# Optimization experiments

Measured on AMD Instinct MI355X. Metric: run time of the kernel, lower is better.

## Reference

```python
import jax, jax.numpy as jnp
import numpy as np

B, L, D = 32, 8192, 1024
KERNEL = 5
PAD = (KERNEL - 1) // 2
UNIT = 2
TOPK = 100  # min(max_num_moments=100, L)


def setup_inputs() -> dict:
    key = jax.random.key(0)
    ks = jax.random.split(key, 8)
    scale = 1.0 / np.sqrt(D)
    return {
        "x": jax.random.normal(ks[0], (B, L, D), dtype=jnp.float32),
        "saliency": jax.random.normal(ks[1], (B, L), dtype=jnp.float32),
        "Wc": jax.random.normal(ks[2], (D, 1), dtype=jnp.float32) * scale,
        "bc": jnp.zeros((1,), dtype=jnp.float32),
        "Ww": jax.random.normal(ks[3], (D, 1), dtype=jnp.float32) * scale,
        "bw": jnp.zeros((1,), dtype=jnp.float32),
        "Wo": jax.random.normal(ks[4], (D, 1), dtype=jnp.float32) * scale,
        "bo": jnp.zeros((1,), dtype=jnp.float32),
    }


def _get_boundary(center_pred, window_pred, offset_pred):
    # center_pred: [B, L]. CenterNet-style 1D NMS: keep only local maxima.
    hmax = jax.lax.reduce_window(
        center_pred, -jnp.inf, jax.lax.max,
        window_dimensions=(1, KERNEL), window_strides=(1, 1),
        padding=[(0, 0), (PAD, PAD)])
    cp = center_pred * (hmax == center_pred).astype(center_pred.dtype)
    scores, inds = jax.lax.top_k(cp, TOPK)                    # [B, K]
    off = jnp.take_along_axis(offset_pred, inds, axis=1)      # [B, K]
    win = jnp.clip(jnp.take_along_axis(window_pred, inds, axis=1), 0.0, None)
    center = jnp.clip(inds.astype(cp.dtype) + off, 0.0, float(L - 1))
    start = jnp.clip(center - win * 0.5, 0.0, float(L - 1)) * UNIT
    end = jnp.clip(center + win * 0.5, 0.0, float(L - 1)) * UNIT + UNIT
    return jnp.stack([start, end, scores], axis=-1)           # [B, K, 3]


def reference(x, saliency, Wc, bc, Ww, bw, Wo, bo):
    mask = (saliency >= 0).astype(x.dtype)                    # [B, L]
    center_pred = jax.nn.sigmoid(jnp.squeeze(x @ Wc + bc, -1)) * mask
    window_pred = jnp.squeeze(x @ Ww + bw, -1)
    offset_pred = jnp.squeeze(x @ Wo + bo, -1)
    return _get_boundary(center_pred, window_pred, offset_pred)
```

## Files before the change

kernel.cpp:

```cpp
#include <hip/hip_runtime.h>
#include <stdint.h>

#define NB 32
#define NL 8192
#define ND 1024
#define NTOPK 100
#define CAND_CAP 3072
#define SUBCAP 1536

#define NBLOCKS 1024
#define NWAVES (NBLOCKS * 4)
#define ROWS_PER_WAVE ((NB * NL) / NWAVES)

__global__ __launch_bounds__(256, 4) void proj_kernel(
    const float* __restrict__ x, const float* __restrict__ sal,
    const float* __restrict__ Wc, const float* __restrict__ bc,
    const float* __restrict__ Ww, const float* __restrict__ bw,
    const float* __restrict__ Wo, const float* __restrict__ bo,
    float* __restrict__ center, float* __restrict__ window_,
    float* __restrict__ offset)
{
    const int wid  = (int)(blockIdx.x * 4u + (threadIdx.x >> 6));
    const int lane = (int)(threadIdx.x & 63u);

    const float4* x4  = (const float4*)x;

    float4 wc[4], ww[4], wo[4];
#pragma unroll
    for (int j = 0; j < 4; ++j) {
        const int k = lane + 64 * j;
        wc[j] = ((const float4*)Wc)[k];
        ww[j] = ((const float4*)Ww)[k];
        wo[j] = ((const float4*)Wo)[k];
    }
    const float bcs = bc[0], bws = bw[0], bos = bo[0];

    float4 b0[4], b1[4], b2[4];
    float s0, s1, s2;

#define LOADROW(BUF, SALV, K)                                              \
    {                                                                      \
        const size_t base = (size_t)(wid + (K) * NWAVES) * (ND / 4);       \
        BUF[0] = x4[base + lane];                                          \
        BUF[1] = x4[base + lane + 64];                                     \
        BUF[2] = x4[base + lane + 128];                                    \
        BUF[3] = x4[base + lane + 192];                                    \
        SALV   = sal[wid + (K) * NWAVES];                                  \
    }

#define COMPROW(BUF, SALV, K)                                              \
    {                                                                      \
        float dc = 0.f, dw = 0.f, dz = 0.f;                                \
        _Pragma("unroll")                                                  \
        for (int j = 0; j < 4; ++j) {                                      \
            dc += BUF[j].x * wc[j].x + BUF[j].y * wc[j].y +                \
                  BUF[j].z * wc[j].z + BUF[j].w * wc[j].w;                 \
            dw += BUF[j].x * ww[j].x + BUF[j].y * ww[j].y +                \
                  BUF[j].z * ww[j].z + BUF[j].w * ww[j].w;                 \
            dz += BUF[j].x * wo[j].x + BUF[j].y * wo[j].y +                \
                  BUF[j].z * wo[j].z + BUF[j].w * wo[j].w;                 \
        }                                                                  \
        _Pragma("unroll")                                                  \
        for (int s = 32; s > 0; s >>= 1) {                                 \
            dc += __shfl_xor(dc, s, 64);                                   \
            dw += __shfl_xor(dw, s, 64);                                   \
            dz += __shfl_xor(dz, s, 64);                                   \
        }                                                                  \
        const int row = wid + (K) * NWAVES;                                \
        if (lane == 0) {                                                   \
            const float m = (SALV >= 0.f) ? 1.f : 0.f;                     \
            center[row] = m / (1.f + expf(-(dc + bcs)));                   \
        } else if (lane == 1) {                                            \
            window_[row] = dw + bws;                                       \
        } else if (lane == 2) {                                            \
            offset[row] = dz + bos;                                        \
        }                                                                  \
    }

    LOADROW(b0, s0, 0)
    LOADROW(b1, s1, 1)

    for (int g = 0; g < 21; ++g) {
        const int k = g * 3;
        LOADROW(b2, s2, k + 2)
        COMPROW(b0, s0, k)
        if (k + 3 < ROWS_PER_WAVE) LOADROW(b0, s0, k + 3)
        COMPROW(b1, s1, k + 1)
        if (k + 4 < ROWS_PER_WAVE) LOADROW(b1, s1, k + 4)
        COMPROW(b2, s2, k + 2)
    }
    COMPROW(b0, s0, 63)

#undef LOADROW
#undef COMPROW
}

__device__ __forceinline__ void emit_one(
    int b, int rank, int idx, float val,
    const float* __restrict__ window_, const float* __restrict__ offset,
    float* __restrict__ out)
{
    const float off = offset[b * NL + idx];
    float win = window_[b * NL + idx];
    win = fmaxf(win, 0.f);
    float c = (float)idx + off;
    c = fminf(fmaxf(c, 0.f), (float)(NL - 1));
    float s = fminf(fmaxf(c - 0.5f * win, 0.f), (float)(NL - 1)) * 2.0f;
    float e = fminf(fmaxf(c + 0.5f * win, 0.f), (float)(NL - 1)) * 2.0f + 2.0f;
    float* o = out + ((size_t)b * NTOPK + rank) * 3;
    o[0] = s;
    o[1] = e;
    o[2] = val;
}

__global__ __launch_bounds__(1024) void topk_kernel(
    const float* __restrict__ center, const float* __restrict__ window_,
    const float* __restrict__ offset, float* __restrict__ out)
{
    __shared__ __align__(16) float c[NL];
    __shared__ unsigned long long cand[CAND_CAP];
    __shared__ int hist[256];
    __shared__ unsigned short sel[SUBCAP];
    __shared__ int cnt, scnt, sB, sAbove, sTH;

    const int b   = blockIdx.x;
    const int tid = (int)threadIdx.x;

    if (tid == 0) { cnt = 0; scnt = 0; }

#pragma unroll
    for (int k = 0; k < NL / 1024; ++k)
        c[tid + k * 1024] = center[b * NL + tid + k * 1024];
    __syncthreads();

#pragma unroll
    for (int k = 0; k < NL / 1024; ++k) {
        const int i = tid + k * 1024;
        const float v = c[i];
        if (v > 0.f) {
            float lm = v;
            if (i >= 2)      lm = fmaxf(lm, c[i - 2]);
            if (i >= 1)      lm = fmaxf(lm, c[i - 1]);
            if (i + 1 < NL)  lm = fmaxf(lm, c[i + 1]);
            if (i + 2 < NL)  lm = fmaxf(lm, c[i + 2]);
            if (v == lm) {
                const int pos = atomicAdd(&cnt, 1);
                if (pos < CAND_CAP) {
                    const unsigned long long key =
                        ((unsigned long long)__float_as_uint(v) << 32) |
                        (unsigned long long)(0xFFFFFFFFu - (unsigned)i);
                    cand[pos] = key;
                }
            }
        }
    }
    __syncthreads();

    const int C = (cnt < CAND_CAP) ? cnt : CAND_CAP;
    bool fullpath = (C <= 2 * NTOPK);

    if (!fullpath) {
        for (int i = tid; i < 256; i += 1024) hist[i] = 0;
        __syncthreads();
        for (int i = tid; i < C; i += 1024) {
            const unsigned u = (unsigned)(cand[i] >> 32);
            atomicAdd(&hist[u >> 22], 1);
        }
        __syncthreads();
        if (tid == 0) {
            int acc = 0, B = 0, above = 0;
            for (int bb = 255; bb >= 0; --bb) {
                acc += hist[bb];
                if (acc >= NTOPK) { B = bb; above = acc - hist[bb]; break; }
            }
            sB = B; sAbove = above;
        }
        __syncthreads();
        const int B = sB, above = sAbove;

        for (int i = tid; i < 256; i += 1024) hist[i] = 0;
        __syncthreads();
        for (int i = tid; i < C; i += 1024) {
            const unsigned u = (unsigned)(cand[i] >> 32);
            if ((int)(u >> 22) == B) atomicAdd(&hist[(u >> 14) & 0xFF], 1);
        }
        __syncthreads();
        if (tid == 0) {
            const int need = NTOPK - above;
            int acc = 0, F = 0;
            for (int fb = 255; fb >= 0; --fb) {
                acc += hist[fb];
                if (acc >= need) { F = fb; break; }
            }
            sTH = (B << 22) | (F << 14);
        }
        __syncthreads();
        const unsigned TH = (unsigned)sTH;

        for (int i = tid; i < C; i += 1024) {
            const unsigned u = (unsigned)(cand[i] >> 32);
            if (u >= TH) {
                const int p = atomicAdd(&scnt, 1);
                if (p < SUBCAP) sel[p] = (unsigned short)i;
            }
        }
        __syncthreads();

        if (scnt > SUBCAP) {
            fullpath = true;
        } else {
            const int S = scnt;
            unsigned long long* subk = (unsigned long long*)c;
            for (int s = tid; s < S; s += 1024) subk[s] = cand[sel[s]];
            __syncthreads();
            for (int s = tid; s < S; s += 1024) {
                const unsigned long long ki = subk[s];
                int r = 0;
                for (int j = 0; j < S; ++j) r += (subk[j] > ki) ? 1 : 0;
                if (r < NTOPK) {
                    const int idx = (int)(0xFFFFFFFFu - (unsigned)(ki & 0xFFFFFFFFull));
                    const float val = __uint_as_float((unsigned)(ki >> 32));
                    emit_one(b, r, idx, val, window_, offset, out);
                }
            }
        }
    }

    if (fullpath) {
        for (int i = tid; i < C; i += 1024) {
            const unsigned long long ki = cand[i];
            int r = 0;
            for (int j = 0; j < C; ++j) r += (cand[j] > ki) ? 1 : 0;
            if (r < NTOPK) {
                const int idx = (int)(0xFFFFFFFFu - (unsigned)(ki & 0xFFFFFFFFull));
                const float val = __uint_as_float((unsigned)(ki >> 32));
                emit_one(b, r, idx, val, window_, offset, out);
            }
        }
        if (C < NTOPK) {
            __syncthreads();
            if (tid == 0) {
                int r = C;
                for (int i = 0; i < NL && r < NTOPK; ++i) {
                    const float v = c[i];
                    bool keep = false;
                    if (v > 0.f) {
                        float lm = v;
                        if (i >= 2)     lm = fmaxf(lm, c[i - 2]);
                        if (i >= 1)     lm = fmaxf(lm, c[i - 1]);
                        if (i + 1 < NL) lm = fmaxf(lm, c[i + 1]);
                        if (i + 2 < NL) lm = fmaxf(lm, c[i + 2]);
                        keep = (v == lm);
                    }
                    if (!keep) {
                        emit_one(b, r, i, 0.f, window_, offset, out);
                        ++r;
                    }
                }
            }
        }
    }
}

extern "C" void kernel_launch(void* const* d_in, const int* in_sizes, int n_in,
                              void* d_out, int out_size, void* d_ws, size_t ws_size,
                              hipStream_t stream)
{
    const float* x   = (const float*)d_in[0];
    const float* sal = (const float*)d_in[1];
    const float* Wc  = (const float*)d_in[2];
    const float* bc  = (const float*)d_in[3];
    const float* Ww  = (const float*)d_in[4];
    const float* bw  = (const float*)d_in[5];
    const float* Wo  = (const float*)d_in[6];
    const float* bo  = (const float*)d_in[7];
    float* out = (float*)d_out;

    float* ws      = (float*)d_ws;
    float* center  = ws;
    float* window_ = ws + NB * NL;
    float* offset  = ws + 2 * NB * NL;

    proj_kernel<<<NBLOCKS, 256, 0, stream>>>(x, sal, Wc, bc, Ww, bw, Wo, bo,
                                             center, window_, offset);

    topk_kernel<<<NB, 1024, 0, stream>>>(center, window_, offset, out);
}
```

Measured before the change: 222.9 us.

## Use wave-aggregated atomics and wave-parallel histogram thresholds in top-k kernel

The top-k kernel now loads the center row with float4 vector loads. It compacts NMS candidates and selected subset keys using ballot/popcount, so each wave does one LDS atomic instead of one per thread. The serial single-thread scans of the radix histograms are replaced by a wave-level prefix-sum search. Selected keys are written straight into the subset buffer, which drops the index indirection and one barrier. The aim is to cut contention and serialization in the top-k stage, but the run is likely dominated by the memory-bound projection kernel.

```diff
diff --git a/kernel.cpp b/kernel.cpp
--- a/kernel.cpp
+++ b/kernel.cpp
@@ -113,6 +113,29 @@
     o[2] = val;
 }
 
+__device__ __forceinline__ void wave_threshold(
+    const int* hist, int K, int ln, int* outB, int* outAbove)
+{
+    const int h0 = hist[4 * ln + 0], h1 = hist[4 * ln + 1];
+    const int h2 = hist[4 * ln + 2], h3 = hist[4 * ln + 3];
+    int S = h0 + h1 + h2 + h3;
+#pragma unroll
+    for (int d = 1; d < 64; d <<= 1) {
+        const int t = __shfl_down(S, d, 64);
+        if (ln + d < 64) S += t;
+    }
+    int Snext = __shfl_down(S, 1, 64);
+    if (ln == 63) Snext = 0;
+    if (S >= K && Snext < K) {
+        int acc = Snext, B = 4 * ln, ab = Snext;
+        if (acc + h3 >= K)                      { B = 4 * ln + 3; ab = acc; }
+        else if (acc + h3 + h2 >= K)            { B = 4 * ln + 2; ab = acc + h3; }
+        else if (acc + h3 + h2 + h1 >= K)       { B = 4 * ln + 1; ab = acc + h3 + h2; }
+        else                                    { B = 4 * ln + 0; ab = acc + h3 + h2 + h1; }
+        *outB = B; *outAbove = ab;
+    }
+}
+
 __global__ __launch_bounds__(1024) void topk_kernel(
     const float* __restrict__ center, const float* __restrict__ window_,
     const float* __restrict__ offset, float* __restrict__ out)
@@ -120,37 +143,43 @@
     __shared__ __align__(16) float c[NL];
     __shared__ unsigned long long cand[CAND_CAP];
     __shared__ int hist[256];
-    __shared__ unsigned short sel[SUBCAP];
     __shared__ int cnt, scnt, sB, sAbove, sTH;
 
     const int b   = blockIdx.x;
     const int tid = (int)threadIdx.x;
+    const int wv  = tid >> 6;
+    const int ln  = tid & 63;
 
     if (tid == 0) { cnt = 0; scnt = 0; }
 
-#pragma unroll
-    for (int k = 0; k < NL / 1024; ++k)
-        c[tid + k * 1024] = center[b * NL + tid + k * 1024];
+    {
+        const float4* src = (const float4*)(center + b * NL);
+        float4* dst = (float4*)c;
+#pragma unroll
+        for (int k = 0; k < NL / 4096; ++k)
+            dst[tid + k * 1024] = src[tid + k * 1024];
+    }
     __syncthreads();
 
 #pragma unroll
     for (int k = 0; k < NL / 1024; ++k) {
         const int i = tid + k * 1024;
         const float v = c[i];
-        if (v > 0.f) {
-            float lm = v;
-            if (i >= 2)      lm = fmaxf(lm, c[i - 2]);
-            if (i >= 1)      lm = fmaxf(lm, c[i - 1]);
-            if (i + 1 < NL)  lm = fmaxf(lm, c[i + 1]);
-            if (i + 2 < NL)  lm = fmaxf(lm, c[i + 2]);
-            if (v == lm) {
-                const int pos = atomicAdd(&cnt, 1);
-                if (pos < CAND_CAP) {
-                    const unsigned long long key =
-                        ((unsigned long long)__float_as_uint(v) << 32) |
-                        (unsigned long long)(0xFFFFFFFFu - (unsigned)i);
-                    cand[pos] = key;
-                }
+        float lm = v;
+        if (i >= 2)      lm = fmaxf(lm, c[i - 2]);
+        if (i >= 1)      lm = fmaxf(lm, c[i - 1]);
+        if (i + 1 < NL)  lm = fmaxf(lm, c[i + 1]);
+        if (i + 2 < NL)  lm = fmaxf(lm, c[i + 2]);
+        const bool keep = (v > 0.f) && (v == lm);
+        const unsigned long long mask = __ballot(keep);
+        int base = 0;
+        if (ln == 0 && mask) base = atomicAdd(&cnt, __popcll(mask));
+        base = __shfl(base, 0, 64);
+        if (keep) {
+            const int pos = base + __popcll(mask & ((1ull << ln) - 1ull));
+            if (pos < CAND_CAP) {
+                cand[pos] = ((unsigned long long)__float_as_uint(v) << 32) |
+                            (unsigned long long)(0xFFFFFFFFu - (unsigned)i);
             }
         }
     }
@@ -160,48 +189,47 @@
     bool fullpath = (C <= 2 * NTOPK);
 
     if (!fullpath) {
-        for (int i = tid; i < 256; i += 1024) hist[i] = 0;
-        __syncthreads();
-        for (int i = tid; i < C; i += 1024) {
-            const unsigned u = (unsigned)(cand[i] >> 32);
-            atomicAdd(&hist[u >> 22], 1);
-        }
-        __syncthreads();
-        if (tid == 0) {
-            int acc = 0, B = 0, above = 0;
-            for (int bb = 255; bb >= 0; --bb) {
-                acc += hist[bb];
-                if (acc >= NTOPK) { B = bb; above = acc - hist[bb]; break; }
-            }
-            sB = B; sAbove = above;
-        }
+        if (tid < 256) hist[tid] = 0;
+        __syncthreads();
+        for (int i = tid; i < C; i += 1024)
+            atomicAdd(&hist[(unsigned)(cand[i] >> 32) >> 22], 1);
+        __syncthreads();
+        if (wv == 0) wave_threshold(hist, NTOPK, ln, &sB, &sAbove);
         __syncthreads();
         const int B = sB, above = sAbove;
 
-        for (int i = tid; i < 256; i += 1024) hist[i] = 0;
+        if (tid < 256) hist[tid] = 0;
         __syncthreads();
         for (int i = tid; i < C; i += 1024) {
             const unsigned u = (unsigned)(cand[i] >> 32);
             if ((int)(u >> 22) == B) atomicAdd(&hist[(u >> 14) & 0xFF], 1);
         }
         __syncthreads();
-        if (tid == 0) {
-            const int need = NTOPK - above;
-            int acc = 0, F = 0;
-            for (int fb = 255; fb >= 0; --fb) {
-                acc += hist[fb];
-                if (acc >= need) { F = fb; break; }
-            }
-            sTH = (B << 22) | (F << 14);
+        if (wv == 0) {
+            int F, dummy;
+            F = 0; dummy = 0;
+            wave_threshold(hist, NTOPK - above, ln, &F, &dummy);
+            if (F != 0 || dummy != 0 || true) {  }
+            int th = (F << 14) | 0;
+            th = (F == 0 && dummy == 0) ? 0 : th;
+#pragma unroll
+            for (int d = 1; d < 64; d <<= 1) th |= __shfl_xor(th, d, 64);
+            if (ln == 0) sTH = (B << 22) | th;
         }
         __syncthreads();
         const unsigned TH = (unsigned)sTH;
 
+        unsigned long long* subk = (unsigned long long*)c;
         for (int i = tid; i < C; i += 1024) {
-            const unsigned u = (unsigned)(cand[i] >> 32);
-            if (u >= TH) {
-                const int p = atomicAdd(&scnt, 1);
-                if (p < SUBCAP) sel[p] = (unsigned short)i;
+            const unsigned long long ki = cand[i];
+            const bool sel = ((unsigned)(ki >> 32) >= TH);
+            const unsigned long long mask = __ballot(sel);
+            int base = 0;
+            if (ln == 0 && mask) base = atomicAdd(&scnt, __popcll(mask));
+            base = __shfl(base, 0, 64);
+            if (sel) {
+                const int p = base + __popcll(mask & ((1ull << ln) - 1ull));
+                if (p < SUBCAP) subk[p] = ki;
             }
         }
         __syncthreads();
@@ -210,11 +238,8 @@
             fullpath = true;
         } else {
             const int S = scnt;
-            unsigned long long* subk = (unsigned long long*)c;
-            for (int s = tid; s < S; s += 1024) subk[s] = cand[sel[s]];
-            __syncthreads();
-            for (int s = tid; s < S; s += 1024) {
-                const unsigned long long ki = subk[s];
+            for (int i = tid; i < S; i += 1024) {
+                const unsigned long long ki = subk[i];
                 int r = 0;
                 for (int j = 0; j < S; ++j) r += (subk[j] > ki) ? 1 : 0;
                 if (r < NTOPK) {
```

Result: faster. 215.0 us (-3.6%).
